# Performance work log

Hardware: AMD Instinct MI355X
Metric: run time of the kernel (lower is better)

Reference implementation:

```python
import jax, jax.numpy as jnp
import numpy as np

# dims: batch, nodes(sensors), window, embed, topk, MLP inter width
B, NODE, WIN, EMB, TOPK, INTER = 256, 512, 64, 64, 16, 512
NEG = 0.2      # LeakyReLU negative slope in GAT attention
EPS = 1e-5     # BatchNorm eps
N = B * NODE   # total graph nodes
E = N * TOPK   # total edges


def _bn(x, gamma, beta, axes):
    # training-mode BatchNorm: batch statistics (biased var), affine gamma/beta
    m = jnp.mean(x, axis=axes, keepdims=True)
    v = jnp.var(x, axis=axes, keepdims=True)
    return (x - m) * jax.lax.rsqrt(v + EPS) * gamma + beta


def setup_inputs() -> dict:
    key = jax.random.key(0)
    ks = jax.random.split(key, 12)
    sd = lambda k, shp, s: jax.random.normal(k, shp, jnp.float32) * s
    return {
        "data": jax.random.normal(ks[0], (B, NODE, WIN), jnp.float32),
        "org_edge_index": jax.random.randint(ks[1], (2, NODE), 0, NODE, dtype=jnp.int32),  # unused by forward
        "W_emb": sd(ks[2], (NODE, EMB), 0.1),          # nn.Embedding weight
        "W_lin": sd(ks[3], (EMB, WIN), 0.1),           # GraphLayer.lin (no bias)
        "att_i": sd(ks[4], (EMB,), 0.1),
        "att_j": sd(ks[5], (EMB,), 0.1),
        "att_em_i": sd(ks[6], (EMB,), 0.1),
        "att_em_j": sd(ks[7], (EMB,), 0.1),
        "b_gnn": jnp.zeros((EMB,), jnp.float32),       # GraphLayer bias
        "g_bn1": jnp.ones((EMB,), jnp.float32), "b_bn1": jnp.zeros((EMB,), jnp.float32),
        "g_bn2": jnp.ones((EMB,), jnp.float32), "b_bn2": jnp.zeros((EMB,), jnp.float32),
        "W1": sd(ks[8], (INTER, EMB), 0.05), "b1": jnp.zeros((INTER,), jnp.float32),
        "g_bn3": jnp.ones((INTER,), jnp.float32), "b_bn3": jnp.zeros((INTER,), jnp.float32),
        "W2": sd(ks[9], (1, INTER), 0.05), "b2": jnp.zeros((1,), jnp.float32),
    }


def reference(data, org_edge_index, W_emb, W_lin, att_i, att_j, att_em_i, att_em_j,
              b_gnn, g_bn1, b_bn1, g_bn2, b_bn2, W1, b1, g_bn3, b_bn3, W2, b2):
    x = data.reshape(N, WIN)

    # ---- graph structure learning: cosine-sim top-k on DETACHED embeddings ----
    w = jax.lax.stop_gradient(W_emb)
    nw = w * jax.lax.rsqrt(jnp.sum(w * w, axis=-1, keepdims=True))
    cos = nw @ nw.T                                  # [NODE, NODE]
    _, topk_idx = jax.lax.top_k(cos, TOPK)           # [NODE, TOPK]; diag==1 -> self in top-k,
                                                     # so remove+add self-loops is a no-op on the edge set
    offs = (jnp.arange(N // NODE) * NODE)[:, None]   # batch offsets
    src = (topk_idx.reshape(-1)[None, :] + offs).reshape(-1)                 # [E] source j
    dst = (jnp.repeat(jnp.arange(NODE), TOPK)[None, :] + offs).reshape(-1)   # [E] target i (sorted)

    # ---- GAT-style message passing (heads=1, concat=False) ----
    xl = x @ W_lin.T                                 # [N, EMB]
    # per-node attention scores for key = [Wx || embedding]
    s_i = xl @ att_i + jnp.tile(W_emb @ att_em_i, B)  # [N]
    s_j = xl @ att_j + jnp.tile(W_emb @ att_em_j, B)  # [N]
    alpha = s_i[dst] + s_j[src]                      # [E]
    alpha = jnp.where(alpha > 0, alpha, NEG * alpha)  # leaky_relu
    # segment softmax over edges grouped by target node
    amax = jax.ops.segment_max(alpha, dst, num_segments=N, indices_are_sorted=True)
    ex = jnp.exp(alpha - amax[dst])
    den = jax.ops.segment_sum(ex, dst, num_segments=N, indices_are_sorted=True)
    attw = ex / den[dst]                             # [E]
    agg = jax.ops.segment_sum(attw[:, None] * xl[src], dst,
                              num_segments=N, indices_are_sorted=True)  # [N, EMB]
    h = jax.nn.relu(_bn(agg + b_gnn, g_bn1, b_bn1, axes=0))             # GNNLayer bn+relu

    # ---- readout: mul by embedding, BN over channels, MLP head (dropout=eval/identity) ----
    z = h.reshape(B, NODE, EMB) * W_emb[None]        # [B, NODE, EMB]
    z = jax.nn.relu(_bn(z, g_bn2, b_bn2, axes=(0, 1)))
    z = jax.nn.relu(_bn(z @ W1.T + b1, g_bn3, b_bn3, axes=(0, 1)))      # [B, NODE, INTER]
    out = (z @ W2.T + b2).reshape(B, NODE)
    return out
```

## Files before the change

### kernel.cpp

```cpp
#include <hip/hip_runtime.h>
#include <hip/hip_bf16.h>

constexpr int BATCH = 256, NNODE = 512, WINW = 64, EMBD = 64, KTOP = 16, CIN = 512;
constexpr int NTOT = BATCH * NNODE;
constexpr float NEGS = 0.2f;
constexpr float EPSBN = 1e-5f;

typedef __attribute__((ext_vector_type(8))) short bf16x8;
typedef __attribute__((ext_vector_type(4))) float f32x4;

union U8 { uint4 u; bf16x8 b; };

__device__ inline float bf2f(unsigned u16) {
  union { unsigned u; float f; } v; v.u = u16 << 16; return v.f;
}
__device__ inline unsigned short f2bf(float x) {
  union { float f; unsigned u; } v; v.f = x;
  unsigned r = v.u + 0x7fff + ((v.u >> 16) & 1);
  return (unsigned short)(r >> 16);
}

__global__ void k_prep(const float* __restrict__ W_emb,
                       const float* __restrict__ att_em_i,
                       const float* __restrict__ att_em_j,
                       float* __restrict__ nw, float* __restrict__ emb_si,
                       float* __restrict__ emb_sj) {
  int i = blockIdx.x, e = threadIdx.x;
  float w  = W_emb[i * EMBD + e];
  float sq = w * w;
  float si = w * att_em_i[e];
  float sj = w * att_em_j[e];
  for (int o = 32; o > 0; o >>= 1) {
    sq += __shfl_xor(sq, o);
    si += __shfl_xor(si, o);
    sj += __shfl_xor(sj, o);
  }
  nw[i * EMBD + e] = w * rsqrtf(sq);
  if (e == 0) { emb_si[i] = si; emb_sj[i] = sj; }
}

__global__ __launch_bounds__(256) void k_topk(const float* __restrict__ nw,
                                              int* __restrict__ topk) {
  __shared__ float nwi[EMBD];
  __shared__ float wbv[4];
  __shared__ int   wbi[4];
  __shared__ int   winner;
  int i = blockIdx.x, t = threadIdx.x, wv = t >> 6, ln = t & 63;
  if (t < EMBD) nwi[t] = nw[i * EMBD + t];
  __syncthreads();
  float v0 = 0.f, v1 = 0.f;
  #pragma unroll
  for (int k = 0; k < EMBD; k++) {
    v0 += nw[t * EMBD + k] * nwi[k];
    v1 += nw[(t + 256) * EMBD + k] * nwi[k];
  }
  for (int sel = 0; sel < KTOP; sel++) {
    float bv; int bi;
    if (v1 > v0) { bv = v1; bi = t + 256; } else { bv = v0; bi = t; }
    #pragma unroll
    for (int o = 1; o < 64; o <<= 1) {
      float ov = __shfl_xor(bv, o);
      int   oi = __shfl_xor(bi, o);
      if (ov > bv || (ov == bv && oi < bi)) { bv = ov; bi = oi; }
    }
    if (ln == 0) { wbv[wv] = bv; wbi[wv] = bi; }
    __syncthreads();
    if (t == 0) {
      float B = wbv[0]; int I = wbi[0];
      #pragma unroll
      for (int w = 1; w < 4; w++)
        if (wbv[w] > B || (wbv[w] == B && wbi[w] < I)) { B = wbv[w]; I = wbi[w]; }
      topk[i * KTOP + sel] = I;
      winner = I;
    }
    __syncthreads();
    int wi = winner;
    if (wi == t) v0 = -3.f;
    else if (wi == t + 256) v1 = -3.f;
  }
}

__global__ __launch_bounds__(1024) void k_fuse(
    const float* __restrict__ data, const float* __restrict__ W_lin,
    const float* __restrict__ att_i, const float* __restrict__ att_j,
    const float* __restrict__ emb_si, const float* __restrict__ emb_sj,
    const int* __restrict__ topk,
    unsigned* __restrict__ aggb, float* __restrict__ gsum1,
    float* __restrict__ gss1) {
  __shared__ float xl[NNODE * EMBD];
  __shared__ float ssi[NNODE];
  __shared__ float ssj[NNODE];
  __shared__ float redb[16 * 128];
  const int b = blockIdx.x;
  const int t = threadIdx.x, w = t >> 6, ln = t & 63;
  const int lm = ln & 15, lq = ln >> 4, kb = lq * 8;

  bf16x8 bfrag[4][2];
  float ai4[4], aj4[4];
  #pragma unroll
  for (int ti = 0; ti < 4; ti++) {
    int ch = ti * 16 + lm;
    ai4[ti] = att_i[ch]; aj4[ti] = att_j[ch];
    #pragma unroll
    for (int s = 0; s < 2; s++) {
      const float* wp = W_lin + ch * WINW + s * 32 + kb;
      float4 w0 = *(const float4*)wp;
      float4 w1 = *(const float4*)(wp + 4);
      bf16x8 f;
      f[0] = (short)f2bf(w0.x); f[1] = (short)f2bf(w0.y);
      f[2] = (short)f2bf(w0.z); f[3] = (short)f2bf(w0.w);
      f[4] = (short)f2bf(w1.x); f[5] = (short)f2bf(w1.y);
      f[6] = (short)f2bf(w1.z); f[7] = (short)f2bf(w1.w);
      bfrag[ti][s] = f;
    }
  }
  #pragma unroll
  for (int tt = 0; tt < 2; tt++) {
    int tile = w * 2 + tt;
    const float* dr = data + ((size_t)b * NNODE + tile * 16 + lm) * WINW + kb;
    f32x4 acc[4];
    #pragma unroll
    for (int ti = 0; ti < 4; ti++) acc[ti] = (f32x4){0.f, 0.f, 0.f, 0.f};
    #pragma unroll
    for (int s = 0; s < 2; s++) {
      float4 d0 = *(const float4*)(dr + s * 32);
      float4 d1 = *(const float4*)(dr + s * 32 + 4);
      bf16x8 af;
      af[0] = (short)f2bf(d0.x); af[1] = (short)f2bf(d0.y);
      af[2] = (short)f2bf(d0.z); af[3] = (short)f2bf(d0.w);
      af[4] = (short)f2bf(d1.x); af[5] = (short)f2bf(d1.y);
      af[6] = (short)f2bf(d1.z); af[7] = (short)f2bf(d1.w);
      #pragma unroll
      for (int ti = 0; ti < 4; ti++)
        acc[ti] = __builtin_amdgcn_mfma_f32_16x16x32_bf16(af, bfrag[ti][s], acc[ti], 0, 0, 0);
    }
    #pragma unroll
    for (int r = 0; r < 4; r++) {
      int nd = tile * 16 + lq * 4 + r;
      float si = 0.f, sj = 0.f;
      #pragma unroll
      for (int ti = 0; ti < 4; ti++) {
        float v = acc[ti][r];
        xl[nd * EMBD + ti * 16 + lm] = v;
        si += v * ai4[ti];
        sj += v * aj4[ti];
      }
      si += __shfl_xor(si, 1); si += __shfl_xor(si, 2);
      si += __shfl_xor(si, 4); si += __shfl_xor(si, 8);
      sj += __shfl_xor(sj, 1); sj += __shfl_xor(sj, 2);
      sj += __shfl_xor(sj, 4); sj += __shfl_xor(sj, 8);
      if (lm == 0) { ssi[nd] = si + emb_si[nd]; ssj[nd] = sj + emb_sj[nd]; }
    }
  }
  __syncthreads();
  const int nd4 = ln >> 4, l4 = ln & 15;
  float psx = 0.f, psy = 0.f, psz = 0.f, psw = 0.f;
  float qsx = 0.f, qsy = 0.f, qsz = 0.f, qsw = 0.f;
  for (int it = 0; it < 8; it++) {
    int node = w * 32 + it * 4 + nd4;
    const int4* tp = (const int4*)(topk + node * KTOP);
    int4 i0 = tp[0], i1 = tp[1], i2 = tp[2], i3 = tp[3];
    int idx[16] = {i0.x, i0.y, i0.z, i0.w, i1.x, i1.y, i1.z, i1.w,
                   i2.x, i2.y, i2.z, i2.w, i3.x, i3.y, i3.z, i3.w};
    float sid = ssi[node];
    float al[16], mx = -1e30f;
    #pragma unroll
    for (int k = 0; k < KTOP; k++) {
      float a = sid + ssj[idx[k]];
      a = a > 0.f ? a : NEGS * a;
      al[k] = a;
      mx = fmaxf(mx, a);
    }
    float den = 0.f;
    #pragma unroll
    for (int k = 0; k < KTOP; k++) { al[k] = __expf(al[k] - mx); den += al[k]; }
    float inv = 1.f / den;
    float ax = 0.f, ay = 0.f, az = 0.f, aw = 0.f;
    #pragma unroll
    for (int k = 0; k < KTOP; k++) {
      float4 v = *(const float4*)&xl[idx[k] * EMBD + l4 * 4];
      ax += al[k] * v.x; ay += al[k] * v.y; az += al[k] * v.z; aw += al[k] * v.w;
    }
    ax *= inv; ay *= inv; az *= inv; aw *= inv;
    unsigned u0 = (unsigned)f2bf(ax) | ((unsigned)f2bf(ay) << 16);
    unsigned u1 = (unsigned)f2bf(az) | ((unsigned)f2bf(aw) << 16);
    *(uint2*)(aggb + (((size_t)b * NNODE + node) << 5) + l4 * 2) = make_uint2(u0, u1);
    psx += ax; psy += ay; psz += az; psw += aw;
    qsx += ax * ax; qsy += ay * ay; qsz += az * az; qsw += aw * aw;
  }
  #pragma unroll
  for (int o = 16; o <= 32; o <<= 1) {
    psx += __shfl_xor(psx, o); psy += __shfl_xor(psy, o);
    psz += __shfl_xor(psz, o); psw += __shfl_xor(psw, o);
    qsx += __shfl_xor(qsx, o); qsy += __shfl_xor(qsy, o);
    qsz += __shfl_xor(qsz, o); qsw += __shfl_xor(qsw, o);
  }
  if (ln < 16) {
    float4 a = {psx, psy, psz, psw};
    float4 q = {qsx, qsy, qsz, qsw};
    *(float4*)&redb[w * 128 + ln * 4] = a;
    *(float4*)&redb[w * 128 + 64 + ln * 4] = q;
  }
  __syncthreads();
  if (t < 64) {
    float s = 0.f;
    #pragma unroll
    for (int w16 = 0; w16 < 16; w16++) s += redb[w16 * 128 + t];
    atomicAdd(&gsum1[t], s);
  } else if (t < 128) {
    int e = t - 64;
    float s = 0.f;
    #pragma unroll
    for (int w16 = 0; w16 < 16; w16++) s += redb[w16 * 128 + 64 + e];
    atomicAdd(&gss1[e], s);
  }
}

__global__ void k_fin(const float* __restrict__ gsum, const float* __restrict__ gss,
                      const float* __restrict__ g, const float* __restrict__ bb,
                      float* __restrict__ a, float* __restrict__ c, int C) {
  int e = blockIdx.x * blockDim.x + threadIdx.x;
  if (e >= C) return;
  const float invn = 1.f / (float)NTOT;
  float m = gsum[e] * invn;
  float v = gss[e] * invn - m * m;
  float aa = g[e] * rsqrtf(v + EPSBN);
  a[e] = aa;
  c[e] = bb[e] - m * aa;
}

__global__ __launch_bounds__(256) void k_zstats2(
    const unsigned* __restrict__ aggb, const float* __restrict__ W_emb,
    const float* __restrict__ a1, const float* __restrict__ c1,
    unsigned* __restrict__ zp, float* __restrict__ gsum2,
    float* __restrict__ gss2) {
  __shared__ float red[4][8][32];
  int t = threadIdx.x;
  int gid = blockIdx.x * 256 + t;
  int p = t & 31;
  int c0 = 2 * p;
  float a10 = a1[c0], a11 = a1[c0 + 1], c10 = c1[c0], c11 = c1[c0 + 1];
  const float2* we2  = (const float2*)W_emb;
  float ps0 = 0.f, ps1 = 0.f, q0 = 0.f, q1 = 0.f;
  int stride = gridDim.x * 256;
  for (int idx = gid; idx < NTOT * 32; idx += stride) {
    unsigned u = aggb[idx];
    float vx = bf2f(u & 0xffffu), vy = bf2f(u >> 16);
    int node = (idx >> 5) & (NNODE - 1);
    float2 w = we2[node * 32 + p];
    float z0 = vx * a10 + c10; z0 = z0 > 0.f ? z0 : 0.f; z0 *= w.x;
    float z1 = vy * a11 + c11; z1 = z1 > 0.f ? z1 : 0.f; z1 *= w.y;
    zp[idx] = (unsigned)f2bf(z0) | ((unsigned)f2bf(z1) << 16);
    ps0 += z0; q0 += z0 * z0; ps1 += z1; q1 += z1 * z1;
  }
  int g = t >> 5;
  red[0][g][p] = ps0; red[1][g][p] = ps1; red[2][g][p] = q0; red[3][g][p] = q1;
  __syncthreads();
  if (t < 128) {
    int v = t >> 5, p2 = t & 31;
    float s = 0.f;
    #pragma unroll
    for (int k = 0; k < 8; k++) s += red[v][k][p2];
    float* dst = (v & 2) ? gss2 : gsum2;
    atomicAdd(&dst[2 * p2 + (v & 1)], s);
  }
}

__global__ __launch_bounds__(256) void k_gram(
    const unsigned* __restrict__ zp, const float* __restrict__ a2,
    const float* __restrict__ c2, float* __restrict__ Gpart,
    float* __restrict__ hpart, unsigned* __restrict__ hb) {
  __shared__ float hst[128 * 68];
  __shared__ float red[4][64];
  const int t = threadIdx.x, wv = t >> 6, ln = t & 63;
  const int i0 = 8 * (ln & 7), j0 = 8 * (ln >> 3);
  const int p = t & 31, c0 = 2 * p;
  float a20 = a2[c0], a21 = a2[c0 + 1], c20 = c2[c0], c21 = c2[c0 + 1];
  float ga[8][8];
  #pragma unroll
  for (int a = 0; a < 8; a++)
    #pragma unroll
    for (int b = 0; b < 8; b++) ga[a][b] = 0.f;
  float hs[8] = {0.f, 0.f, 0.f, 0.f, 0.f, 0.f, 0.f, 0.f};
  const int rowbase = blockIdx.x * 256;
  for (int st = 0; st < 2; st++) {
    int base32 = (rowbase + st * 128) * 32;
    unsigned us[16];
    #pragma unroll
    for (int s = 0; s < 16; s++) us[s] = zp[base32 + s * 256 + t];
    __syncthreads();
    #pragma unroll
    for (int s = 0; s < 16; s++) {
      int row = s * 8 + (t >> 5);
      float z0 = bf2f(us[s] & 0xffffu);
      float z1 = bf2f(us[s] >> 16);
      float h0 = z0 * a20 + c20; h0 = h0 > 0.f ? h0 : 0.f;
      float h1 = z1 * a21 + c21; h1 = h1 > 0.f ? h1 : 0.f;
      *(float2*)&hst[row * 68 + c0] = make_float2(h0, h1);
      hb[(size_t)(rowbase + st * 128 + row) * 32 + p] =
          (unsigned)f2bf(h0) | ((unsigned)f2bf(h1) << 16);
    }
    __syncthreads();
    for (int q = 0; q < 32; q++) {
      int r = wv * 32 + q;
      float4 hi0 = *(const float4*)&hst[r * 68 + i0];
      float4 hi1 = *(const float4*)&hst[r * 68 + i0 + 4];
      float4 hj0 = *(const float4*)&hst[r * 68 + j0];
      float4 hj1 = *(const float4*)&hst[r * 68 + j0 + 4];
      float hia[8] = {hi0.x, hi0.y, hi0.z, hi0.w, hi1.x, hi1.y, hi1.z, hi1.w};
      float hja[8] = {hj0.x, hj0.y, hj0.z, hj0.w, hj1.x, hj1.y, hj1.z, hj1.w};
      #pragma unroll
      for (int a = 0; a < 8; a++) {
        float hv = hia[a];
        hs[a] += hv;
        #pragma unroll
        for (int b = 0; b < 8; b++) ga[a][b] += hv * hja[b];
      }
    }
  }
  __syncthreads();
  float* G_lds = hst;
  for (int k = t; k < 4096; k += 256) G_lds[k] = 0.f;
  __syncthreads();
  for (int w = 0; w < 4; w++) {
    if (wv == w) {
      #pragma unroll
      for (int a = 0; a < 8; a++)
        #pragma unroll
        for (int bb = 0; bb < 8; bb++) {
          int b = (bb + (ln & 7)) & 7;
          G_lds[(i0 + a) * 64 + j0 + b] += ga[a][b];
        }
    }
    __syncthreads();
  }
  for (int k = t; k < 4096; k += 256) Gpart[(size_t)blockIdx.x * 4096 + k] = G_lds[k];
  #pragma unroll
  for (int k = 0; k < 8; k++) {
    float v = hs[k];
    v += __shfl_xor(v, 8); v += __shfl_xor(v, 16); v += __shfl_xor(v, 32);
    hs[k] = v * 0.125f;
  }
  if (ln < 8) {
    #pragma unroll
    for (int k = 0; k < 8; k++) red[wv][ln * 8 + k] = hs[k];
  }
  __syncthreads();
  if (t < 64)
    hpart[(size_t)blockIdx.x * 64 + t] = red[0][t] + red[1][t] + red[2][t] + red[3][t];
}

__global__ __launch_bounds__(256) void k_gred(const float* __restrict__ Gpart,
                                              const float* __restrict__ hpart,
                                              float* __restrict__ G,
                                              float* __restrict__ hsum) {
  int wi = blockIdx.x * 256 + threadIdx.x;
  if (wi < 32768) {
    int e = wi & 4095, seg = wi >> 12;
    float s = 0.f;
    #pragma unroll 8
    for (int k = 0; k < 64; k++) s += Gpart[(size_t)((seg << 6) + k) * 4096 + e];
    atomicAdd(&G[e], s);
  } else {
    int wi2 = wi - 32768;
    int e = wi2 & 63, seg = wi2 >> 6;
    float s = 0.f;
    #pragma unroll 8
    for (int k = 0; k < 64; k++) s += hpart[(size_t)((seg << 6) + k) * 64 + e];
    atomicAdd(&hsum[e], s);
  }
}

__global__ __launch_bounds__(64) void k_fin3q(
    const float* __restrict__ G, const float* __restrict__ hsum,
    const float* __restrict__ W1, const float* __restrict__ b1,
    const float* __restrict__ g3, const float* __restrict__ b3,
    float* __restrict__ a3, float* __restrict__ c3) {
  __shared__ float sw[64];
  int c = blockIdx.x, i = threadIdx.x;
  float w1i = W1[c * 64 + i];
  sw[i] = w1i;
  __syncthreads();
  float gw = 0.f;
  #pragma unroll
  for (int j = 0; j < 64; j++) gw += G[j * 64 + i] * sw[j];
  float t1 = w1i * gw;
  float t2 = w1i * hsum[i];
  for (int o = 32; o > 0; o >>= 1) { t1 += __shfl_xor(t1, o); t2 += __shfl_xor(t2, o); }
  if (i == 0) {
    float b1c = b1[c];
    const float fn = (float)NTOT, invn = 1.f / fn;
    float sum3 = t2 + fn * b1c;
    float ss3  = t1 + 2.f * b1c * t2 + fn * b1c * b1c;
    float m = sum3 * invn;
    float v = ss3 * invn - m * m;
    float aa = g3[c] * rsqrtf(v + EPSBN);
    a3[c] = aa;
    c3[c] = b3[c] - m * aa;
  }
}

__global__ __launch_bounds__(512) void k_gout3(
    const unsigned* __restrict__ hb, const float* __restrict__ W1,
    const float* __restrict__ b1, const float* __restrict__ a3,
    const float* __restrict__ c3, const float* __restrict__ W2,
    const float* __restrict__ b2, float* __restrict__ out) {
  const int t = threadIdx.x, wv = t >> 6, ln = t & 63;
  const int lm = ln & 15, lq = ln >> 4, kb = lq * 8;
  bf16x8 bfrag[4][2];
  float b1c[4], a3c[4], c3c[4], w2c[4];
  #pragma unroll
  for (int nt = 0; nt < 4; nt++) {
    int col = wv * 64 + nt * 16 + lm;
    b1c[nt] = b1[col]; a3c[nt] = a3[col]; c3c[nt] = c3[col]; w2c[nt] = W2[col];
    #pragma unroll
    for (int s = 0; s < 2; s++) {
      const float* wp = W1 + col * EMBD + s * 32 + kb;
      float4 w0 = *(const float4*)wp;
      float4 w1 = *(const float4*)(wp + 4);
      bf16x8 f;
      f[0] = (short)f2bf(w0.x); f[1] = (short)f2bf(w0.y);
      f[2] = (short)f2bf(w0.z); f[3] = (short)f2bf(w0.w);
      f[4] = (short)f2bf(w1.x); f[5] = (short)f2bf(w1.y);
      f[6] = (short)f2bf(w1.z); f[7] = (short)f2bf(w1.w);
      bfrag[nt][s] = f;
    }
  }
  float b2v = b2[0];
  const uint4* h4 = (const uint4*)hb;
  for (int tile = blockIdx.x; tile < NTOT / 16; tile += gridDim.x) {
    int rowbase = tile * 16;
    U8 ua, ub;
    ua.u = h4[(size_t)(rowbase + lm) * 8 + lq];
    ub.u = h4[(size_t)(rowbase + lm) * 8 + 4 + lq];
    f32x4 acc[4];
    #pragma unroll
    for (int nt = 0; nt < 4; nt++) acc[nt] = (f32x4){0.f, 0.f, 0.f, 0.f};
    #pragma unroll
    for (int nt = 0; nt < 4; nt++)
      acc[nt] = __builtin_amdgcn_mfma_f32_16x16x32_bf16(ua.b, bfrag[nt][0], acc[nt], 0, 0, 0);
    #pragma unroll
    for (int nt = 0; nt < 4; nt++)
      acc[nt] = __builtin_amdgcn_mfma_f32_16x16x32_bf16(ub.b, bfrag[nt][1], acc[nt], 0, 0, 0);
    #pragma unroll
    for (int r = 0; r < 4; r++) {
      float p = 0.f;
      #pragma unroll
      for (int nt = 0; nt < 4; nt++) {
        float z2 = acc[nt][r] + b1c[nt];
        float y = z2 * a3c[nt] + c3c[nt];
        y = y > 0.f ? y : 0.f;
        p += y * w2c[nt];
      }
      p += __shfl_xor(p, 1); p += __shfl_xor(p, 2);
      p += __shfl_xor(p, 4); p += __shfl_xor(p, 8);
      if (lm == 0) {
        if (wv == 0) p += b2v;
        atomicAdd(&out[rowbase + lq * 4 + r], p);
      }
    }
  }
}

extern "C" void kernel_launch(void* const* d_in, const int* in_sizes, int n_in,
                              void* d_out, int out_size, void* d_ws, size_t ws_size,
                              hipStream_t stream) {
  const float* data     = (const float*)d_in[0];
  const float* W_emb    = (const float*)d_in[2];
  const float* W_lin    = (const float*)d_in[3];
  const float* att_i    = (const float*)d_in[4];
  const float* att_j    = (const float*)d_in[5];
  const float* att_em_i = (const float*)d_in[6];
  const float* att_em_j = (const float*)d_in[7];
  const float* g_bn1    = (const float*)d_in[9];
  const float* b_bn1    = (const float*)d_in[10];
  const float* g_bn2    = (const float*)d_in[11];
  const float* b_bn2    = (const float*)d_in[12];
  const float* W1       = (const float*)d_in[13];
  const float* b1       = (const float*)d_in[14];
  const float* g_bn3    = (const float*)d_in[15];
  const float* b_bn3    = (const float*)d_in[16];
  const float* W2       = (const float*)d_in[17];
  const float* b2       = (const float*)d_in[18];
  float* out = (float*)d_out;

  char* p = (char*)d_ws;
  auto alloc = [&](size_t bytes) {
    void* r = (void*)p;
    p += (bytes + 255) & ~(size_t)255;
    return r;
  };
  unsigned* aggb  = (unsigned*)alloc((size_t)NTOT * EMBD * 2);
  unsigned* zb    = (unsigned*)alloc((size_t)NTOT * EMBD * 2);
  unsigned* hb    = (unsigned*)alloc((size_t)NTOT * EMBD * 2);
  float*    Gpart = (float*)alloc((size_t)512 * 4096 * 4);
  float*    hpart = (float*)alloc((size_t)512 * 64 * 4);
  float*    nw    = (float*)alloc((size_t)NNODE * EMBD * 4);
  float*    emb_si = (float*)alloc(NNODE * 4);
  float*    emb_sj = (float*)alloc(NNODE * 4);
  int*      topk   = (int*)alloc(NNODE * KTOP * 4);
  float*    stats  = (float*)alloc(4416 * 4);
  float*    coefs  = (float*)alloc(1280 * 4);

  float* gsum1 = stats;       float* gss1 = stats + 64;
  float* gsum2 = stats + 128; float* gss2 = stats + 192;
  float* G     = stats + 256; float* hsum = stats + 4352;
  float* a1 = coefs;       float* c1 = coefs + 64;
  float* a2 = coefs + 128; float* c2 = coefs + 192;
  float* a3 = coefs + 256; float* c3 = coefs + 768;

  hipMemsetAsync(stats, 0, 4416 * 4, stream);
  hipMemsetAsync(out, 0, (size_t)NTOT * 4, stream);

  k_prep<<<NNODE, 64, 0, stream>>>(W_emb, att_em_i, att_em_j, nw, emb_si, emb_sj);
  k_topk<<<NNODE, 256, 0, stream>>>(nw, topk);
  k_fuse<<<BATCH, 1024, 0, stream>>>(data, W_lin, att_i, att_j, emb_si, emb_sj,
                                     topk, aggb, gsum1, gss1);
  k_fin<<<1, 64, 0, stream>>>(gsum1, gss1, g_bn1, b_bn1, a1, c1, EMBD);
  k_zstats2<<<1024, 256, 0, stream>>>(aggb, W_emb, a1, c1, zb, gsum2, gss2);
  k_fin<<<1, 64, 0, stream>>>(gsum2, gss2, g_bn2, b_bn2, a2, c2, EMBD);
  k_gram<<<512, 256, 0, stream>>>(zb, a2, c2, Gpart, hpart, hb);
  k_gred<<<130, 256, 0, stream>>>(Gpart, hpart, G, hsum);
  k_fin3q<<<CIN, 64, 0, stream>>>(G, hsum, W1, b1, g_bn3, b_bn3, a3, c3);
  k_gout3<<<512, 512, 0, stream>>>(hb, W1, b1, a3, c3, W2, b2, out);
}
```

Before: 283.0 us.

## Split GAT fuse kernel, recompute z in gram, use MFMA for Gram matrix

The monolithic 1024-thread per-batch fuse kernel, which held 128KB+ of LDS, is split into two kernels. The first computes the projection xl (stored as bf16) and the attention scores. The second does the edge softmax and aggregation with 256-thread blocks, giving better occupancy and more blocks. The z intermediate is no longer written to global memory; the gram kernel recomputes z and h from aggb. The Gram matrix and column sums now come from bf16 MFMA instead of scalar FMA accumulation. The split adds a global round trip for xl and s_i/s_j and introduces bf16 rounding of xl before aggregation.

```diff
diff --git a/kernel.cpp b/kernel.cpp
--- a/kernel.cpp
+++ b/kernel.cpp
@@ -80,18 +80,12 @@
   }
 }
 
-__global__ __launch_bounds__(1024) void k_fuse(
+__global__ __launch_bounds__(256) void k_xl(
     const float* __restrict__ data, const float* __restrict__ W_lin,
     const float* __restrict__ att_i, const float* __restrict__ att_j,
     const float* __restrict__ emb_si, const float* __restrict__ emb_sj,
-    const int* __restrict__ topk,
-    unsigned* __restrict__ aggb, float* __restrict__ gsum1,
-    float* __restrict__ gss1) {
-  __shared__ float xl[NNODE * EMBD];
-  __shared__ float ssi[NNODE];
-  __shared__ float ssj[NNODE];
-  __shared__ float redb[16 * 128];
-  const int b = blockIdx.x;
+    unsigned* __restrict__ xlb, float* __restrict__ s_i, float* __restrict__ s_j) {
+  __shared__ unsigned short ht[4][16 * 72];
   const int t = threadIdx.x, w = t >> 6, ln = t & 63;
   const int lm = ln & 15, lq = ln >> 4, kb = lq * 8;
 
@@ -114,10 +108,12 @@
       bfrag[ti][s] = f;
     }
   }
+  uint4* xlb4 = (uint4*)xlb;
+  const uint4* hp4 = (const uint4*)&ht[w][0];
   #pragma unroll
   for (int tt = 0; tt < 2; tt++) {
-    int tile = w * 2 + tt;
-    const float* dr = data + ((size_t)b * NNODE + tile * 16 + lm) * WINW + kb;
+    int tile = blockIdx.x * 8 + w * 2 + tt;
+    const float* dr = data + (size_t)(tile * 16 + lm) * WINW + kb;
     f32x4 acc[4];
     #pragma unroll
     for (int ti = 0; ti < 4; ti++) acc[ti] = (f32x4){0.f, 0.f, 0.f, 0.f};
@@ -136,12 +132,13 @@
     }
     #pragma unroll
     for (int r = 0; r < 4; r++) {
-      int nd = tile * 16 + lq * 4 + r;
+      int ndl = lq * 4 + r;
+      int nd = tile * 16 + ndl;
       float si = 0.f, sj = 0.f;
       #pragma unroll
       for (int ti = 0; ti < 4; ti++) {
         float v = acc[ti][r];
-        xl[nd * EMBD + ti * 16 + lm] = v;
+        ht[w][ndl * 72 + ti * 16 + lm] = f2bf(v);
         si += v * ai4[ti];
         sj += v * aj4[ti];
       }
@@ -149,24 +146,49 @@
       si += __shfl_xor(si, 4); si += __shfl_xor(si, 8);
       sj += __shfl_xor(sj, 1); sj += __shfl_xor(sj, 2);
       sj += __shfl_xor(sj, 4); sj += __shfl_xor(sj, 8);
-      if (lm == 0) { ssi[nd] = si + emb_si[nd]; ssj[nd] = sj + emb_sj[nd]; }
-    }
-  }
-  __syncthreads();
+      if (lm == 0) {
+        int node = nd & (NNODE - 1);
+        s_i[nd] = si + emb_si[node];
+        s_j[nd] = sj + emb_sj[node];
+      }
+    }
+    #pragma unroll
+    for (int g = 0; g < 2; g++) {
+      int slot = g * 64 + ln;
+      int row = slot >> 3, grp = slot & 7;
+      xlb4[(size_t)(tile * 16 + row) * 8 + grp] = hp4[row * 9 + grp];
+    }
+  }
+}
+
+__global__ __launch_bounds__(256) void k_edge(
+    const unsigned* __restrict__ xlb, const float* __restrict__ s_i,
+    const float* __restrict__ s_j, const int* __restrict__ topk,
+    unsigned* __restrict__ aggb, float* __restrict__ gsum1,
+    float* __restrict__ gss1) {
+  __shared__ float redb[4][128];
+  const int t = threadIdx.x, w = t >> 6, ln = t & 63;
   const int nd4 = ln >> 4, l4 = ln & 15;
-  float psx = 0.f, psy = 0.f, psz = 0.f, psw = 0.f;
-  float qsx = 0.f, qsy = 0.f, qsz = 0.f, qsw = 0.f;
-  for (int it = 0; it < 8; it++) {
-    int node = w * 32 + it * 4 + nd4;
-    const int4* tp = (const int4*)(topk + node * KTOP);
+  const int b = blockIdx.x & 255;
+  const int seg = blockIdx.x >> 8;
+  const int boff = b * NNODE;
+  const int nbase = seg * 64 + w * 16;
+  const uint2* xl2 = (const uint2*)xlb;
+  uint2* ag2 = (uint2*)aggb;
+  float ps0 = 0.f, ps1 = 0.f, ps2 = 0.f, ps3 = 0.f;
+  float qs0 = 0.f, qs1 = 0.f, qs2 = 0.f, qs3 = 0.f;
+  for (int it = 0; it < 4; it++) {
+    int nl = nbase + it * 4 + nd4;
+    int n = boff + nl;
+    const int4* tp = (const int4*)(topk + nl * KTOP);
     int4 i0 = tp[0], i1 = tp[1], i2 = tp[2], i3 = tp[3];
     int idx[16] = {i0.x, i0.y, i0.z, i0.w, i1.x, i1.y, i1.z, i1.w,
                    i2.x, i2.y, i2.z, i2.w, i3.x, i3.y, i3.z, i3.w};
-    float sid = ssi[node];
+    float sid = s_i[n];
     float al[16], mx = -1e30f;
     #pragma unroll
     for (int k = 0; k < KTOP; k++) {
-      float a = sid + ssj[idx[k]];
+      float a = sid + s_j[boff + idx[k]];
       a = a > 0.f ? a : NEGS * a;
       al[k] = a;
       mx = fmaxf(mx, a);
@@ -178,41 +200,39 @@
     float ax = 0.f, ay = 0.f, az = 0.f, aw = 0.f;
     #pragma unroll
     for (int k = 0; k < KTOP; k++) {
-      float4 v = *(const float4*)&xl[idx[k] * EMBD + l4 * 4];
-      ax += al[k] * v.x; ay += al[k] * v.y; az += al[k] * v.z; aw += al[k] * v.w;
+      uint2 v = xl2[(size_t)(boff + idx[k]) * 16 + l4];
+      ax += al[k] * bf2f(v.x & 0xffffu);
+      ay += al[k] * bf2f(v.x >> 16);
+      az += al[k] * bf2f(v.y & 0xffffu);
+      aw += al[k] * bf2f(v.y >> 16);
     }
     ax *= inv; ay *= inv; az *= inv; aw *= inv;
-    unsigned u0 = (unsigned)f2bf(ax) | ((unsigned)f2bf(ay) << 16);
-    unsigned u1 = (unsigned)f2bf(az) | ((unsigned)f2bf(aw) << 16);
-    *(uint2*)(aggb + (((size_t)b * NNODE + node) << 5) + l4 * 2) = make_uint2(u0, u1);
-    psx += ax; psy += ay; psz += az; psw += aw;
-    qsx += ax * ax; qsy += ay * ay; qsz += az * az; qsw += aw * aw;
+    uint2 st;
+    st.x = (unsigned)f2bf(ax) | ((unsigned)f2bf(ay) << 16);
+    st.y = (unsigned)f2bf(az) | ((unsigned)f2bf(aw) << 16);
+    ag2[(size_t)n * 16 + l4] = st;
+    ps0 += ax; ps1 += ay; ps2 += az; ps3 += aw;
+    qs0 += ax * ax; qs1 += ay * ay; qs2 += az * az; qs3 += aw * aw;
   }
   #pragma unroll
   for (int o = 16; o <= 32; o <<= 1) {
-    psx += __shfl_xor(psx, o); psy += __shfl_xor(psy, o);
-    psz += __shfl_xor(psz, o); psw += __shfl_xor(psw, o);
-    qsx += __shfl_xor(qsx, o); qsy += __shfl_xor(qsy, o);
-    qsz += __shfl_xor(qsz, o); qsw += __shfl_xor(qsw, o);
+    ps0 += __shfl_xor(ps0, o); ps1 += __shfl_xor(ps1, o);
+    ps2 += __shfl_xor(ps2, o); ps3 += __shfl_xor(ps3, o);
+    qs0 += __shfl_xor(qs0, o); qs1 += __shfl_xor(qs1, o);
+    qs2 += __shfl_xor(qs2, o); qs3 += __shfl_xor(qs3, o);
   }
   if (ln < 16) {
-    float4 a = {psx, psy, psz, psw};
-    float4 q = {qsx, qsy, qsz, qsw};
-    *(float4*)&redb[w * 128 + ln * 4] = a;
-    *(float4*)&redb[w * 128 + 64 + ln * 4] = q;
+    float4 a = {ps0, ps1, ps2, ps3};
+    float4 q = {qs0, qs1, qs2, qs3};
+    *(float4*)&redb[w][ln * 4] = a;
+    *(float4*)&redb[w][64 + ln * 4] = q;
   }
   __syncthreads();
   if (t < 64) {
-    float s = 0.f;
-    #pragma unroll
-    for (int w16 = 0; w16 < 16; w16++) s += redb[w16 * 128 + t];
-    atomicAdd(&gsum1[t], s);
+    atomicAdd(&gsum1[t], redb[0][t] + redb[1][t] + redb[2][t] + redb[3][t]);
   } else if (t < 128) {
     int e = t - 64;
-    float s = 0.f;
-    #pragma unroll
-    for (int w16 = 0; w16 < 16; w16++) s += redb[w16 * 128 + 64 + e];
-    atomicAdd(&gss1[e], s);
+    atomicAdd(&gss1[e], redb[0][64 + e] + redb[1][64 + e] + redb[2][64 + e] + redb[3][64 + e]);
   }
 }
 
@@ -229,11 +249,10 @@
   c[e] = bb[e] - m * aa;
 }
 
-__global__ __launch_bounds__(256) void k_zstats2(
+__global__ __launch_bounds__(256) void k_zstats3(
     const unsigned* __restrict__ aggb, const float* __restrict__ W_emb,
     const float* __restrict__ a1, const float* __restrict__ c1,
-    unsigned* __restrict__ zp, float* __restrict__ gsum2,
-    float* __restrict__ gss2) {
+    float* __restrict__ gsum2, float* __restrict__ gss2) {
   __shared__ float red[4][8][32];
   int t = threadIdx.x;
   int gid = blockIdx.x * 256 + t;
@@ -250,7 +269,6 @@
     float2 w = we2[node * 32 + p];
     float z0 = vx * a10 + c10; z0 = z0 > 0.f ? z0 : 0.f; z0 *= w.x;
     float z1 = vy * a11 + c11; z1 = z1 > 0.f ? z1 : 0.f; z1 *= w.y;
-    zp[idx] = (unsigned)f2bf(z0) | ((unsigned)f2bf(z1) << 16);
     ps0 += z0; q0 += z0 * z0; ps1 += z1; q1 += z1 * z1;
   }
   int g = t >> 5;
@@ -266,88 +284,121 @@
   }
 }
 
-__global__ __launch_bounds__(256) void k_gram(
-    const unsigned* __restrict__ zp, const float* __restrict__ a2,
-    const float* __restrict__ c2, float* __restrict__ Gpart,
-    float* __restrict__ hpart, unsigned* __restrict__ hb) {
-  __shared__ float hst[128 * 68];
-  __shared__ float red[4][64];
+__global__ __launch_bounds__(256) void k_gram2(
+    const unsigned* __restrict__ aggb, const float* __restrict__ W_emb,
+    const float* __restrict__ a1, const float* __restrict__ c1,
+    const float* __restrict__ a2, const float* __restrict__ c2,
+    float* __restrict__ Gpart, float* __restrict__ hpart,
+    unsigned* __restrict__ hb) {
+  __shared__ float smem[4 * 4480];
+  __shared__ float hred[4][64];
   const int t = threadIdx.x, wv = t >> 6, ln = t & 63;
-  const int i0 = 8 * (ln & 7), j0 = 8 * (ln >> 3);
-  const int p = t & 31, c0 = 2 * p;
-  float a20 = a2[c0], a21 = a2[c0 + 1], c20 = c2[c0], c21 = c2[c0 + 1];
-  float ga[8][8];
-  #pragma unroll
-  for (int a = 0; a < 8; a++)
-    #pragma unroll
-    for (int b = 0; b < 8; b++) ga[a][b] = 0.f;
-  float hs[8] = {0.f, 0.f, 0.f, 0.f, 0.f, 0.f, 0.f, 0.f};
-  const int rowbase = blockIdx.x * 256;
-  for (int st = 0; st < 2; st++) {
-    int base32 = (rowbase + st * 128) * 32;
-    unsigned us[16];
-    #pragma unroll
-    for (int s = 0; s < 16; s++) us[s] = zp[base32 + s * 256 + t];
-    __syncthreads();
-    #pragma unroll
-    for (int s = 0; s < 16; s++) {
-      int row = s * 8 + (t >> 5);
-      float z0 = bf2f(us[s] & 0xffffu);
-      float z1 = bf2f(us[s] >> 16);
-      float h0 = z0 * a20 + c20; h0 = h0 > 0.f ? h0 : 0.f;
-      float h1 = z1 * a21 + c21; h1 = h1 > 0.f ? h1 : 0.f;
-      *(float2*)&hst[row * 68 + c0] = make_float2(h0, h1);
-      hb[(size_t)(rowbase + st * 128 + row) * 32 + p] =
-          (unsigned)f2bf(h0) | ((unsigned)f2bf(h1) << 16);
-    }
-    __syncthreads();
-    for (int q = 0; q < 32; q++) {
-      int r = wv * 32 + q;
-      float4 hi0 = *(const float4*)&hst[r * 68 + i0];
-      float4 hi1 = *(const float4*)&hst[r * 68 + i0 + 4];
-      float4 hj0 = *(const float4*)&hst[r * 68 + j0];
-      float4 hj1 = *(const float4*)&hst[r * 68 + j0 + 4];
-      float hia[8] = {hi0.x, hi0.y, hi0.z, hi0.w, hi1.x, hi1.y, hi1.z, hi1.w};
-      float hja[8] = {hj0.x, hj0.y, hj0.z, hj0.w, hj1.x, hj1.y, hj1.z, hj1.w};
-      #pragma unroll
-      for (int a = 0; a < 8; a++) {
-        float hv = hia[a];
-        hs[a] += hv;
+  const int lm = ln & 15, lq = ln >> 4;
+  const int r4 = ln & 7, ch8 = ln >> 3;
+  const int c0 = ch8 * 8;
+  float a1v[8], c1v[8], a2v[8], c2v[8];
+  #pragma unroll
+  for (int j = 0; j < 8; j++) {
+    a1v[j] = a1[c0 + j]; c1v[j] = c1[c0 + j];
+    a2v[j] = a2[c0 + j]; c2v[j] = c2[c0 + j];
+  }
+  unsigned* ht = (unsigned*)(smem + wv * 4480);
+  bf16x8 ones;
+  #pragma unroll
+  for (int j = 0; j < 8; j++) ones[j] = (short)0x3F80;
+  f32x4 acc[4][4];
+  f32x4 accS[4];
+  #pragma unroll
+  for (int i = 0; i < 4; i++) {
+    accS[i] = (f32x4){0.f, 0.f, 0.f, 0.f};
+    #pragma unroll
+    for (int j = 0; j < 4; j++) acc[i][j] = (f32x4){0.f, 0.f, 0.f, 0.f};
+  }
+  const uint4* ab4 = (const uint4*)aggb;
+  uint4* hb4 = (uint4*)hb;
+  const float4* we4 = (const float4*)W_emb;
+  const int blockrow = blockIdx.x * 256;
+  #pragma unroll
+  for (int ck = 0; ck < 2; ck++) {
+    int k0 = blockrow + wv * 64 + ck * 32;
+    #pragma unroll
+    for (int rr2 = 0; rr2 < 2; rr2++) {
+      float h2[2][8];
+      #pragma unroll
+      for (int rh = 0; rh < 2; rh++) {
+        int lr = r4 * 4 + rr2 * 2 + rh;
+        int row = k0 + lr;
+        int node = row & (NNODE - 1);
+        uint4 u = ab4[(size_t)row * 8 + ch8];
+        float4 w0 = we4[node * 16 + ch8 * 2];
+        float4 w1 = we4[node * 16 + ch8 * 2 + 1];
+        float gv[8] = {bf2f(u.x & 0xffffu), bf2f(u.x >> 16),
+                       bf2f(u.y & 0xffffu), bf2f(u.y >> 16),
+                       bf2f(u.z & 0xffffu), bf2f(u.z >> 16),
+                       bf2f(u.w & 0xffffu), bf2f(u.w >> 16)};
+        float wv8[8] = {w0.x, w0.y, w0.z, w0.w, w1.x, w1.y, w1.z, w1.w};
+        uint hp[4];
         #pragma unroll
-        for (int b = 0; b < 8; b++) ga[a][b] += hv * hja[b];
+        for (int j = 0; j < 8; j++) {
+          float z = gv[j] * a1v[j] + c1v[j];
+          z = z > 0.f ? z : 0.f;
+          z *= wv8[j];
+          float hh = z * a2v[j] + c2v[j];
+          hh = hh > 0.f ? hh : 0.f;
+          h2[rh][j] = hh;
+        }
+        #pragma unroll
+        for (int j = 0; j < 4; j++)
+          hp[j] = (unsigned)f2bf(h2[rh][2 * j]) | ((unsigned)f2bf(h2[rh][2 * j + 1]) << 16);
+        hb4[(size_t)row * 8 + ch8] = make_uint4(hp[0], hp[1], hp[2], hp[3]);
       }
+      #pragma unroll
+      for (int cc = 0; cc < 8; cc++) {
+        int ch = c0 + cc;
+        int base = ch * 20 + ((ch >> 3) & 3) * 4;
+        ht[base + r4 * 2 + rr2] =
+            (unsigned)f2bf(h2[0][cc]) | ((unsigned)f2bf(h2[1][cc]) << 16);
+      }
+    }
+    bf16x8 frag[4];
+    #pragma unroll
+    for (int i = 0; i < 4; i++) {
+      int ch = i * 16 + lm;
+      int base = ch * 20 + ((ch >> 3) & 3) * 4;
+      frag[i] = *(const bf16x8*)(ht + base + lq * 4);
+    }
+    #pragma unroll
+    for (int i = 0; i < 4; i++) {
+      #pragma unroll
+      for (int j = 0; j < 4; j++)
+        acc[i][j] = __builtin_amdgcn_mfma_f32_16x16x32_bf16(frag[i], frag[j], acc[i][j], 0, 0, 0);
+      accS[i] = __builtin_amdgcn_mfma_f32_16x16x32_bf16(frag[i], ones, accS[i], 0, 0, 0);
     }
   }
   __syncthreads();
-  float* G_lds = hst;
-  for (int k = t; k < 4096; k += 256) G_lds[k] = 0.f;
+  float* Gb = smem + wv * 4480;
+  #pragma unroll
+  for (int i = 0; i < 4; i++) {
+    #pragma unroll
+    for (int j = 0; j < 4; j++) {
+      float4 vv = {acc[i][j][0], acc[i][j][1], acc[i][j][2], acc[i][j][3]};
+      *(float4*)(Gb + (j * 16 + lm) * 68 + i * 16 + lq * 4) = vv;
+    }
+    if (lm == 0) {
+      float4 sv = {accS[i][0], accS[i][1], accS[i][2], accS[i][3]};
+      *(float4*)&hred[wv][i * 16 + lq * 4] = sv;
+    }
+  }
   __syncthreads();
-  for (int w = 0; w < 4; w++) {
-    if (wv == w) {
-      #pragma unroll
-      for (int a = 0; a < 8; a++)
-        #pragma unroll
-        for (int bb = 0; bb < 8; bb++) {
-          int b = (bb + (ln & 7)) & 7;
-          G_lds[(i0 + a) * 64 + j0 + b] += ga[a][b];
-        }
-    }
-    __syncthreads();
-  }
-  for (int k = t; k < 4096; k += 256) Gpart[(size_t)blockIdx.x * 4096 + k] = G_lds[k];
-  #pragma unroll
-  for (int k = 0; k < 8; k++) {
-    float v = hs[k];
-    v += __shfl_xor(v, 8); v += __shfl_xor(v, 16); v += __shfl_xor(v, 32);
-    hs[k] = v * 0.125f;
-  }
-  if (ln < 8) {
-    #pragma unroll
-    for (int k = 0; k < 8; k++) red[wv][ln * 8 + k] = hs[k];
-  }
-  __syncthreads();
+  for (int k = t; k < 4096; k += 256) {
+    int col = k >> 6, row = k & 63;
+    int o = col * 68 + row;
+    Gpart[(size_t)blockIdx.x * 4096 + k] =
+        smem[o] + smem[4480 + o] + smem[2 * 4480 + o] + smem[3 * 4480 + o];
+  }
   if (t < 64)
-    hpart[(size_t)blockIdx.x * 64 + t] = red[0][t] + red[1][t] + red[2][t] + red[3][t];
+    hpart[(size_t)blockIdx.x * 64 + t] =
+        hred[0][t] + hred[1][t] + hred[2][t] + hred[3][t];
 }
 
 __global__ __launch_bounds__(256) void k_gred(const float* __restrict__ Gpart,
@@ -491,10 +542,12 @@
     return r;
   };
   unsigned* aggb  = (unsigned*)alloc((size_t)NTOT * EMBD * 2);
-  unsigned* zb    = (unsigned*)alloc((size_t)NTOT * EMBD * 2);
+  unsigned* xlb   = (unsigned*)alloc((size_t)NTOT * EMBD * 2);
   unsigned* hb    = (unsigned*)alloc((size_t)NTOT * EMBD * 2);
   float*    Gpart = (float*)alloc((size_t)512 * 4096 * 4);
   float*    hpart = (float*)alloc((size_t)512 * 64 * 4);
+  float*    s_i   = (float*)alloc((size_t)NTOT * 4);
+  float*    s_j   = (float*)alloc((size_t)NTOT * 4);
   float*    nw    = (float*)alloc((size_t)NNODE * EMBD * 4);
   float*    emb_si = (float*)alloc(NNODE * 4);
   float*    emb_sj = (float*)alloc(NNODE * 4);
@@ -514,12 +567,13 @@
 
   k_prep<<<NNODE, 64, 0, stream>>>(W_emb, att_em_i, att_em_j, nw, emb_si, emb_sj);
   k_topk<<<NNODE, 256, 0, stream>>>(nw, topk);
-  k_fuse<<<BATCH, 1024, 0, stream>>>(data, W_lin, att_i, att_j, emb_si, emb_sj,
-                                     topk, aggb, gsum1, gss1);
+  k_xl<<<1024, 256, 0, stream>>>(data, W_lin, att_i, att_j, emb_si, emb_sj,
+                                 xlb, s_i, s_j);
+  k_edge<<<2048, 256, 0, stream>>>(xlb, s_i, s_j, topk, aggb, gsum1, gss1);
   k_fin<<<1, 64, 0, stream>>>(gsum1, gss1, g_bn1, b_bn1, a1, c1, EMBD);
-  k_zstats2<<<1024, 256, 0, stream>>>(aggb, W_emb, a1, c1, zb, gsum2, gss2);
+  k_zstats3<<<1024, 256, 0, stream>>>(aggb, W_emb, a1, c1, gsum2, gss2);
   k_fin<<<1, 64, 0, stream>>>(gsum2, gss2, g_bn2, b_bn2, a2, c2, EMBD);
-  k_gram<<<512, 256, 0, stream>>>(zb, a2, c2, Gpart, hpart, hb);
+  k_gram2<<<512, 256, 0, stream>>>(aggb, W_emb, a1, c1, a2, c2, Gpart, hpart, hb);
   k_gred<<<130, 256, 0, stream>>>(Gpart, hpart, G, hsum);
   k_fin3q<<<CIN, 64, 0, stream>>>(G, hsum, W1, b1, g_bn3, b_bn3, a3, c3);
   k_gout3<<<512, 512, 0, stream>>>(hb, W1, b1, a3, c3, W2, b2, out);
```

Result: slower. 309.5 us (+9.3%).
